# Performance work log

Measured on AMD Instinct MI355X. Metric: run time of the kernel, lower is better.

## Reference

```python
import jax, jax.numpy as jnp
import numpy as np

B, L, H = 512, 10, 256   # batch dialogs, max context len (=dia_len), hidden_size
D = 2 * H                # utt encoding dim (bidirectional)
E = 0.01                 # self.e
BN_EPS = 1e-5


def _linear(x, w, b):
    return x @ w.T + b


def _bn(x, g, b):
    # BatchNorm2d over channel dim 1 of [B, L, L, hid]; training-mode batch stats.
    m = jnp.mean(x, axis=(0, 2, 3), keepdims=True)
    v = jnp.mean((x - m) ** 2, axis=(0, 2, 3), keepdims=True)
    return (x - m) / jnp.sqrt(v + BN_EPS) * g[None, :, None, None] + b[None, :, None, None]


def setup_inputs() -> dict:
    key = jax.random.key(0)
    ks = jax.random.split(key, 24)
    u = lambda k, s: jax.random.uniform(k, s, jnp.float32, -0.02, 0.02)
    n = lambda k, s: jax.random.normal(k, s, jnp.float32) * 0.05
    inp = {
        'utt_encs': jax.random.normal(ks[0], (B, L, D), jnp.float32),
        'aij_eps': jax.random.normal(ks[1], (B, L, L), jnp.float32),
        'sij_eps': jax.random.normal(ks[2], (B, L, L), jnp.float32),
        'context_lens': jax.random.randint(ks[3], (B,), 2, L + 1),
        # mlp_aij_mij: Linear(4H->H), BN, ReLU, Linear(H->H), BN, ReLU, Linear(H->1)
        'a_w1': u(ks[4], (H, 2 * D)), 'a_b1': jnp.zeros((H,)),
        'a_g1': jnp.ones((L,)), 'a_be1': jnp.zeros((L,)),
        'a_w2': u(ks[5], (H, H)), 'a_b2': jnp.zeros((H,)),
        'a_g2': jnp.ones((L,)), 'a_be2': jnp.zeros((L,)),
        'a_w3': u(ks[6], (1, H)), 'a_b3': jnp.zeros((1,)),
        # mlp_sij: Linear(4H->H), BN, Tanh, Linear(H->H), BN, Tanh
        's_w1': u(ks[7], (H, 2 * D)), 's_b1': jnp.zeros((H,)),
        's_g1': jnp.ones((L,)), 's_be1': jnp.zeros((L,)),
        's_w2': u(ks[8], (H, H)), 's_b2': jnp.zeros((H,)),
        's_g2': jnp.ones((L,)), 's_be2': jnp.zeros((L,)),
        'mu_w': u(ks[9], (1, H)), 'mu_b': jnp.zeros((1,)),
        'sg_w': u(ks[10], (1, H)), 'sg_b': jnp.zeros((1,)),
        # update_hidden_state: GRU(2H -> H), single step
        'gru_wi': n(ks[11], (3 * H, D)), 'gru_wh': n(ks[12], (3 * H, H)),
        'gru_bi': jnp.zeros((3 * H,)), 'gru_bh': jnp.zeros((3 * H,)),
    }
    return inp


def reference(utt_encs, aij_eps, sij_eps, context_lens,
              a_w1, a_b1, a_g1, a_be1, a_w2, a_b2, a_g2, a_be2, a_w3, a_b3,
              s_w1, s_b1, s_g1, s_be1, s_w2, s_b2, s_g2, s_be2,
              mu_w, mu_b, sg_w, sg_b, gru_wi, gru_wh, gru_bi, gru_bh):
    # pairwise concat [B, L, L, 4H]
    x_ij = jnp.concatenate([
        jnp.broadcast_to(utt_encs[:, :, None, :], (B, L, L, D)),
        jnp.broadcast_to(utt_encs[:, None, :, :], (B, L, L, D)),
    ], axis=-1)
    # aij branch
    h1 = jax.nn.relu(_bn(_linear(x_ij, a_w1, a_b1), a_g1, a_be1))
    h2 = jax.nn.relu(_bn(_linear(h1, a_w2, a_b2), a_g2, a_be2))
    aij_mij = _linear(h2, a_w3, a_b3)[..., 0]                      # [B, L, L]
    aij_mu = jax.nn.softplus(aij_mij) + E
    aij_std = jnp.sqrt(jax.nn.softplus((1.0 - aij_mu) * aij_mu) + E)
    aij = jax.nn.softplus(aij_eps * aij_std + aij_mu) + E
    # sij branch
    t1 = jnp.tanh(_bn(_linear(x_ij, s_w1, s_b1), s_g1, s_be1))
    sij_latent = jnp.tanh(_bn(_linear(t1, s_w2, s_b2), s_g2, s_be2))
    sij_mu = _linear(sij_latent, mu_w, mu_b)[..., 0]
    sij_sigma = _linear(sij_latent, sg_w, sg_b)[..., 0]
    sij = sij_eps * jnp.sqrt(aij * sij_sigma * sij_sigma) + aij * sij_mu
    wij = aij * sij                                                # [B, L, L]
    # per-dialog aggregation (vectorized): anchor = context_lens - 1,
    # neighbors are j < anchor (anchor row, anchor excluded, j <= num_neighbours)
    anchor = context_lens - 1                                      # [B]
    w_row = jnp.take_along_axis(wij, anchor[:, None, None], axis=1)[:, 0, :]  # [B, L]
    mask = jnp.arange(L)[None, :] < anchor[:, None]
    logits = jnp.where(mask, w_row, -jnp.inf)
    p = jax.nn.softmax(logits, axis=-1)
    p = jnp.where(mask, p, 0.0)
    message = jnp.einsum('bj,bjd->bd', p, utt_encs)                # [B, 2H]
    ue_a = jnp.take_along_axis(utt_encs, anchor[:, None, None], axis=1)[:, 0, :]
    h0 = ue_a[:, :H] + ue_a[:, H:]                                 # [B, H]
    # single GRU step (torch GRU cell math)
    gi = message @ gru_wi.T + gru_bi
    gh = h0 @ gru_wh.T + gru_bh
    i_r, i_z, i_n = jnp.split(gi, 3, axis=-1)
    h_r, h_z, h_n = jnp.split(gh, 3, axis=-1)
    r = jax.nn.sigmoid(i_r + h_r)
    z = jax.nn.sigmoid(i_z + h_z)
    ncand = jnp.tanh(i_n + r * h_n)
    return (1.0 - z) * ncand + z * h0                              # [B, H]
```

## Files before the change

### kernel.cpp

```cpp
#include <hip/hip_runtime.h>
#include <math.h>


typedef __attribute__((ext_vector_type(8))) short short8;
typedef __attribute__((ext_vector_type(4))) float f32x4;

__device__ __forceinline__ float softplusf(float x) {
  return x > 0.f ? x + log1pf(expf(-x)) : log1pf(expf(x));
}
__device__ __forceinline__ float wred64(float v) {
#pragma unroll
  for (int o = 32; o > 0; o >>= 1) v += __shfl_down(v, o);
  return v;
}
__device__ __forceinline__ unsigned short f2bf(float f) {
  unsigned int u = __float_as_uint(f);
  u += 0x7fffu + ((u >> 16) & 1u);
  return (unsigned short)(u >> 16);
}
__device__ __forceinline__ float bf2f(unsigned short u) {
  return __uint_as_float(((unsigned int)u) << 16);
}
__device__ __forceinline__ short8 pack8(const float* __restrict__ p) {
  float4 v0 = *(const float4*)p;
  float4 v1 = *(const float4*)(p + 4);
  short8 r;
  r[0] = (short)f2bf(v0.x); r[1] = (short)f2bf(v0.y);
  r[2] = (short)f2bf(v0.z); r[3] = (short)f2bf(v0.w);
  r[4] = (short)f2bf(v1.x); r[5] = (short)f2bf(v1.y);
  r[6] = (short)f2bf(v1.z); r[7] = (short)f2bf(v1.w);
  return r;
}

__global__ __launch_bounds__(256) void prep_weights(
    const float* __restrict__ utt,
    const float* __restrict__ a_w1, const float* __restrict__ s_w1,
    const float* __restrict__ a_w2, const float* __restrict__ s_w2,
    const float* __restrict__ gru_wi, const float* __restrict__ gru_wh,
    unsigned short* __restrict__ Af, unsigned short* __restrict__ Bf,
    unsigned short* __restrict__ W2fa, unsigned short* __restrict__ W2fs,
    unsigned short* __restrict__ wibf, unsigned short* __restrict__ whbf) {
  int i = blockIdx.x * 256 + threadIdx.x;
  if (i < 327680) {
    int lane = i & 63, ks = (i >> 6) & 15, rb = i >> 10;
    int row = rb * 16 + (lane & 15);
    int k = ks * 32 + (lane >> 4) * 8;
    *(short8*)&Af[i * 8] = pack8(&utt[row * 512 + k]);
    return;
  }
  i -= 327680;
  if (i < 65536) {
    int lane = i & 63, cf = (i >> 6) & 3, ks = (i >> 8) & 15, cb = i >> 12;
    int c = cb * 64 + cf * 16 + (lane & 15);
    int k = ks * 32 + (lane >> 4) * 8;
    const float* src;
    if (c < 256)       src = &a_w1[c * 1024 + k];
    else if (c < 512)  src = &a_w1[(c - 256) * 1024 + 512 + k];
    else if (c < 768)  src = &s_w1[(c - 512) * 1024 + k];
    else               src = &s_w1[(c - 768) * 1024 + 512 + k];
    *(short8*)&Bf[i * 8] = pack8(src);
    return;
  }
  i -= 65536;
  if (i < 8192) {
    int lane = i & 63, cf = (i >> 6) & 3, ks = (i >> 8) & 7, cb = i >> 11;
    int c = cb * 64 + cf * 16 + (lane & 15);
    int k = ks * 32 + (lane >> 4) * 8;
    *(short8*)&W2fa[i * 8] = pack8(&a_w2[c * 256 + k]);
    return;
  }
  i -= 8192;
  if (i < 8192) {
    int lane = i & 63, cf = (i >> 6) & 3, ks = (i >> 8) & 7, cb = i >> 11;
    int c = cb * 64 + cf * 16 + (lane & 15);
    int k = ks * 32 + (lane >> 4) * 8;
    *(short8*)&W2fs[i * 8] = pack8(&s_w2[c * 256 + k]);
    return;
  }
  i -= 8192;
  if (i < 49152) { *(short8*)&wibf[i * 8] = pack8(&gru_wi[i * 8]); return; }
  i -= 49152;
  *(short8*)&whbf[i * 8] = pack8(&gru_wh[i * 8]);
}

__global__ __launch_bounds__(256) void gemm_pq_swz(
    const unsigned short* __restrict__ Af, const unsigned short* __restrict__ Bf,
    unsigned short* __restrict__ C) {
  int t = threadIdx.x;
  int w = t >> 6, l = t & 63, li = l & 15, lg = l >> 4;
  int rb0 = blockIdx.x * 4;
  int cb = blockIdx.y * 4 + w;
  const unsigned short* Bb = Bf + cb * (16 * 4 * 512);
  f32x4 acc[4][4] = {};
  short8 acur[4], bcur[4], anxt[4], bnxt[4];
#pragma unroll
  for (int fr = 0; fr < 4; ++fr) acur[fr] = *(const short8*)&Af[((rb0 + fr) * 16 + 0) * 512 + l * 8];
#pragma unroll
  for (int cf = 0; cf < 4; ++cf) bcur[cf] = *(const short8*)&Bb[(0 * 4 + cf) * 512 + l * 8];
  for (int ks = 0; ks < 16; ++ks) {
    if (ks < 15) {
#pragma unroll
      for (int fr = 0; fr < 4; ++fr) anxt[fr] = *(const short8*)&Af[((rb0 + fr) * 16 + ks + 1) * 512 + l * 8];
#pragma unroll
      for (int cf = 0; cf < 4; ++cf) bnxt[cf] = *(const short8*)&Bb[((ks + 1) * 4 + cf) * 512 + l * 8];
    }
#pragma unroll
    for (int fr = 0; fr < 4; ++fr)
#pragma unroll
      for (int cf = 0; cf < 4; ++cf)
        acc[fr][cf] = __builtin_amdgcn_mfma_f32_16x16x32_bf16(acur[fr], bcur[cf], acc[fr][cf], 0, 0, 0);
#pragma unroll
    for (int fr = 0; fr < 4; ++fr) acur[fr] = anxt[fr];
#pragma unroll
    for (int cf = 0; cf < 4; ++cf) bcur[cf] = bnxt[cf];
  }
  int rowBase = blockIdx.x * 64, colBase = cb * 64;
#pragma unroll
  for (int fr = 0; fr < 4; ++fr)
#pragma unroll
    for (int reg = 0; reg < 4; ++reg) {
      int r = rowBase + fr * 16 + lg * 4 + reg;
      unsigned short* crow = C + r * 1024 + colBase + li;
#pragma unroll
      for (int cf = 0; cf < 4; ++cf) crow[cf * 16] = f2bf(acc[fr][cf][reg]);
    }
}

__global__ __launch_bounds__(256) void stats_kernel(
    const unsigned short* __restrict__ PQ, const float* __restrict__ a_b1,
    const float* __restrict__ s_b1, float* __restrict__ Part) {
  __shared__ float lbins[4][32];
  int b = blockIdx.x, br = blockIdx.y, t = threadIdx.x;
  int w = t >> 6, l = t & 63;
  const unsigned short* base = PQ + b * 10240 + (br ? 512 : 0);
  const float* b1 = br ? s_b1 : a_b1;
  float P[10], Q[10];
#pragma unroll
  for (int j = 0; j < 10; ++j) Q[j] = bf2f(base[j * 1024 + 256 + t]);
#pragma unroll
  for (int i = 0; i < 10; ++i) P[i] = bf2f(base[i * 1024 + t]);
  float sq = 0.f, sq2 = 0.f;
#pragma unroll
  for (int j = 0; j < 10; ++j) { sq += Q[j]; sq2 += Q[j] * Q[j]; }
  float qbar = sq * 0.1f;
  float bb1 = b1[t];
  float r;
  r = wred64(sq);  if (l == 0) lbins[w][0] = r;
  r = wred64(sq2); if (l == 0) lbins[w][1] = r;
#pragma unroll
  for (int i = 0; i < 10; ++i) {
    float a = P[i] + bb1;
    r = wred64(P[i]);     if (l == 0) lbins[w][2 + i * 3] = r;
    r = wred64(a * a);    if (l == 0) lbins[w][3 + i * 3] = r;
    r = wred64(a * qbar); if (l == 0) lbins[w][4 + i * 3] = r;
  }
  __syncthreads();
  if (t < 32) Part[(b * 2 + br) * 32 + t] = lbins[0][t] + lbins[1][t] + lbins[2][t] + lbins[3][t];
}

__global__ void reduce_bn1(const float* __restrict__ Part,
                           const float* __restrict__ a_b1, const float* __restrict__ s_b1,
                           const float* __restrict__ a_g1, const float* __restrict__ a_be1,
                           const float* __restrict__ s_g1, const float* __restrict__ s_be1,
                           float* __restrict__ ST) {
  __shared__ float tmp[256];
  __shared__ float mom[32];
  int br = blockIdx.x, t = threadIdx.x;
  int v = t & 31, c = t >> 5;
  float s = 0.f;
  for (int b = c * 64; b < c * 64 + 64; ++b) s += Part[(b * 2 + br) * 32 + v];
  tmp[t] = s;
  __syncthreads();
  if (t < 32) {
    float m = 0.f;
#pragma unroll
    for (int k = 0; k < 8; ++k) m += tmp[k * 32 + t];
    mom[t] = m;
  }
  __syncthreads();
  if (t < 10) {
    int i = t;
    const float* b1 = br ? s_b1 : a_b1;
    float bsum = 0.f;
    for (int h = 0; h < 256; ++h) bsum += b1[h];
    float meanb1 = bsum * (1.f / 256.f);
    const float invBH = 1.f / (512.f * 256.f);
    const float invBLH = 1.f / (512.f * 10.f * 256.f);
    float SP = mom[2 + i * 3], SA2 = mom[3 + i * 3], SPQ = mom[4 + i * 3];
    float SQ = mom[0], SQ2 = mom[1];
    float mean = SP * invBH + meanb1 + SQ * invBLH;
    float Ez2 = SA2 * invBH + 2.f * SPQ * invBH + SQ2 * invBLH;
    float var = Ez2 - mean * mean;
    float g = br ? s_g1[i] : a_g1[i];
    float be = br ? s_be1[i] : a_be1[i];
    float sc = g / sqrtf(var + 1e-5f);
    ST[64 + br * 20 + i] = sc;
    ST[64 + br * 20 + 10 + i] = be - mean * sc;
  }
}

__global__ __launch_bounds__(256, 4) void fused_layer2_half(
    const unsigned short* __restrict__ PQ, const float* __restrict__ ST,
    const float* __restrict__ a_b1, const float* __restrict__ s_b1,
    const unsigned short* __restrict__ W2fa, const unsigned short* __restrict__ W2fs,
    const float* __restrict__ a_b2, const float* __restrict__ s_b2,
    const int* __restrict__ cl, unsigned short* __restrict__ Z2a, unsigned short* __restrict__ Z2s,
    float* __restrict__ Part2) {
  __shared__ __align__(16) unsigned short Atile[64][264];
  __shared__ float bins[10];
  int b = blockIdx.x, half = blockIdx.y, br = blockIdx.z;
  int i0 = half * 5;
  int p_off = br ? 512 : 0;
  const float* b1 = br ? s_b1 : a_b1;
  const unsigned short* W2f = br ? W2fs : W2fa;
  const float* b2 = br ? s_b2 : a_b2;
  unsigned short* Z2out = br ? Z2s : Z2a;
  int sc_off = br ? 84 : 64;
  int t = threadIdx.x;
  int anc = cl[b] - 1;
  if (t < 10) bins[t] = 0.f;
  int w = t >> 6, l = t & 63, li = l & 15, lg = l >> 4;
  int colBase = w * 64;
  const unsigned short* Wb = W2f + w * (8 * 4 * 512);
  short8 bcur[4], bnxt[4];
#pragma unroll
  for (int cf = 0; cf < 4; ++cf) bcur[cf] = *(const short8*)&Wb[(0 * 4 + cf) * 512 + l * 8];
  float b2v[4];
#pragma unroll
  for (int cf = 0; cf < 4; ++cf) b2v[cf] = b2[colBase + cf * 16 + li];
  for (int idx = t; idx < 14 * 264; idx += 256) (&Atile[50][0])[idx] = 0;
  {
    int c = t;
    float b1c = b1[c];
    float P[5], Q[10];
#pragma unroll
    for (int j = 0; j < 10; ++j) Q[j] = bf2f(PQ[(b * 10 + j) * 1024 + p_off + 256 + c]);
#pragma unroll
    for (int il = 0; il < 5; ++il) P[il] = bf2f(PQ[(b * 10 + i0 + il) * 1024 + p_off + c]);
#pragma unroll
    for (int il = 0; il < 5; ++il) {
      float sc = ST[sc_off + i0 + il], sh = ST[sc_off + 10 + i0 + il];
      float base = (P[il] + b1c) * sc + sh;
#pragma unroll
      for (int j = 0; j < 10; ++j) {
        float z = base + Q[j] * sc;
        float h;
        if (br) {
          float ex = __expf(2.f * z);
          h = (ex - 1.f) / (ex + 1.f);
        } else {
          h = fmaxf(z, 0.f);
        }
        Atile[il * 10 + j][c] = f2bf(h);
      }
    }
  }
  __syncthreads();
  f32x4 acc[4][4] = {};
  for (int ks = 0; ks < 8; ++ks) {
    if (ks < 7) {
#pragma unroll
      for (int cf = 0; cf < 4; ++cf) bnxt[cf] = *(const short8*)&Wb[((ks + 1) * 4 + cf) * 512 + l * 8];
    }
    int ka = ks * 32 + lg * 8;
#pragma unroll
    for (int fr = 0; fr < 4; ++fr) {
      short8 afr = *(const short8*)&Atile[fr * 16 + li][ka];
#pragma unroll
      for (int cf = 0; cf < 4; ++cf)
        acc[fr][cf] = __builtin_amdgcn_mfma_f32_16x16x32_bf16(afr, bcur[cf], acc[fr][cf], 0, 0, 0);
    }
#pragma unroll
    for (int cf = 0; cf < 4; ++cf) bcur[cf] = bnxt[cf];
  }
#pragma unroll
  for (int fr = 0; fr < 4; ++fr) {
#pragma unroll
    for (int reg = 0; reg < 4; ++reg) {
      int row = fr * 16 + lg * 4 + reg;
      bool valid = row < 50;
      int il = row / 10, jj = row - il * 10;
      float z0 = acc[fr][0][reg] + b2v[0];
      float z1 = acc[fr][1][reg] + b2v[1];
      float z2 = acc[fr][2][reg] + b2v[2];
      float z3 = acc[fr][3][reg] + b2v[3];
      if (valid && (i0 + il) == anc) {
        unsigned short* dst = Z2out + (b * 10 + jj) * 256 + colBase + li;
        dst[0] = f2bf(z0); dst[16] = f2bf(z1); dst[32] = f2bf(z2); dst[48] = f2bf(z3);
      }
      float s = valid ? (z0 + z1 + z2 + z3) : 0.f;
      float q = valid ? (z0 * z0 + z1 * z1 + z2 * z2 + z3 * z3) : 0.f;
#pragma unroll
      for (int o = 1; o < 16; o <<= 1) {
        s += __shfl_xor(s, o);
        q += __shfl_xor(q, o);
      }
      if (li == 0 && valid) {
        atomicAdd(&bins[il], s);
        atomicAdd(&bins[5 + il], q);
      }
    }
  }
  __syncthreads();
  if (t < 5) {
    Part2[(br * 10 + i0 + t) * 512 + b] = bins[t];
    Part2[10240 + (br * 10 + i0 + t) * 512 + b] = bins[5 + t];
  }
}

__global__ __launch_bounds__(256) void finalize_bn2(
    const float* __restrict__ Part2,
    const float* __restrict__ a_g2, const float* __restrict__ a_be2,
    const float* __restrict__ s_g2, const float* __restrict__ s_be2,
    float* __restrict__ ST) {
  int t = threadIdx.x;
  int w = t >> 6, l = t & 63;
#pragma unroll
  for (int pp = 0; pp < 5; ++pp) {
    int p = w * 5 + pp;
    float s = 0.f, q = 0.f;
#pragma unroll
    for (int k = 0; k < 8; ++k) {
      s += Part2[p * 512 + l + k * 64];
      q += Part2[10240 + p * 512 + l + k * 64];
    }
    s = wred64(s);
    q = wred64(q);
    if (l == 0) {
      int br = p / 10, i = p - br * 10;
      const float invN = 1.f / (512.f * 10.f * 256.f);
      float m = s * invN;
      float v = q * invN - m * m;
      float g = br ? s_g2[i] : a_g2[i];
      float be = br ? s_be2[i] : a_be2[i];
      float sc = g / sqrtf(v + 1e-5f);
      ST[144 + br * 20 + i] = sc;
      ST[144 + br * 20 + 10 + i] = be - m * sc;
    }
  }
}

__global__ __launch_bounds__(256) void gemm_gru2(
    const unsigned short* __restrict__ A0, const unsigned short* __restrict__ B0,
    float* __restrict__ C0, const float* __restrict__ bias0,
    const unsigned short* __restrict__ A1, const unsigned short* __restrict__ B1,
    float* __restrict__ C1, const float* __restrict__ bias1) {
  const unsigned short* A; const unsigned short* Bw; float* C; const float* bias; int K;
  if (blockIdx.z == 0) { A = A0; Bw = B0; C = C0; bias = bias0; K = 512; }
  else                 { A = A1; Bw = B1; C = C1; bias = bias1; K = 256; }
  int t = threadIdx.x;
  int w = t >> 6, l = t & 63, li = l & 15, lg = l >> 4;
  int rowBase = blockIdx.x * 32;
  int colBase = blockIdx.y * 256 + w * 64;
  f32x4 acc[2][4] = {};
  const unsigned short* Arow[2];
  const unsigned short* Brow[4];
#pragma unroll
  for (int fr = 0; fr < 2; ++fr) Arow[fr] = A + (rowBase + fr * 16 + li) * K;
#pragma unroll
  for (int cf = 0; cf < 4; ++cf) Brow[cf] = Bw + (colBase + cf * 16 + li) * K;
  for (int ks = 0; ks < K / 32; ++ks) {
    int ka = ks * 32 + lg * 8;
    short8 afr[2], bfr[4];
#pragma unroll
    for (int fr = 0; fr < 2; ++fr) afr[fr] = *(const short8*)&Arow[fr][ka];
#pragma unroll
    for (int cf = 0; cf < 4; ++cf) bfr[cf] = *(const short8*)&Brow[cf][ka];
#pragma unroll
    for (int fr = 0; fr < 2; ++fr)
#pragma unroll
      for (int cf = 0; cf < 4; ++cf)
        acc[fr][cf] = __builtin_amdgcn_mfma_f32_16x16x32_bf16(afr[fr], bfr[cf], acc[fr][cf], 0, 0, 0);
  }
  float b2v[4];
#pragma unroll
  for (int cf = 0; cf < 4; ++cf) b2v[cf] = bias[colBase + cf * 16 + li];
#pragma unroll
  for (int fr = 0; fr < 2; ++fr)
#pragma unroll
    for (int reg = 0; reg < 4; ++reg) {
      int r = rowBase + fr * 16 + lg * 4 + reg;
      float* crow = C + r * 768 + colBase + li;
#pragma unroll
      for (int cf = 0; cf < 4; ++cf) crow[cf * 16] = acc[fr][cf][reg] + b2v[cf];
    }
}

__global__ __launch_bounds__(256) void postproc_kernel(
    const unsigned short* __restrict__ Z2a, const unsigned short* __restrict__ Z2s,
    const float* __restrict__ ST,
    const float* __restrict__ a_w3, const float* __restrict__ a_b3,
    const float* __restrict__ mu_w, const float* __restrict__ mu_b,
    const float* __restrict__ sg_w, const float* __restrict__ sg_b,
    const float* __restrict__ aij_eps, const float* __restrict__ sij_eps,
    const int* __restrict__ cl, const float* __restrict__ utt,
    unsigned short* __restrict__ msgbf, unsigned short* __restrict__ h0bf,
    float* __restrict__ h0out) {
  int b = blockIdx.x, t = threadIdx.x;
  int w = t >> 6, l = t & 63;
  int a = cl[b] - 1;
  float sc2a = ST[144 + a], sh2a = ST[154 + a];
  float sc2s = ST[164 + a], sh2s = ST[174 + a];
  __shared__ float red[30];
#pragma unroll
  for (int m = 0; m < 3; ++m) {
    int j = w + 4 * m;
    if (j < 10) {
      float pa = 0.f, pm = 0.f, ps = 0.f;
#pragma unroll
      for (int cc = 0; cc < 4; ++cc) {
        int c = l + cc * 64;
        float za = bf2f(Z2a[(b * 10 + j) * 256 + c]);
        float va = fmaxf(za * sc2a + sh2a, 0.f);
        float zs = bf2f(Z2s[(b * 10 + j) * 256 + c]);
        float vs = tanhf(zs * sc2s + sh2s);
        pa += va * a_w3[c];
        pm += vs * mu_w[c];
        ps += vs * sg_w[c];
      }
      pa = wred64(pa); pm = wred64(pm); ps = wred64(ps);
      if (l == 0) { red[j] = pa; red[10 + j] = pm; red[20 + j] = ps; }
    }
  }
  __syncthreads();
  __shared__ float pw[10];
  __shared__ float wijs[16];
  if (t < 10) {
    int j = t;
    float amij = red[j] + a_b3[0];
    float amu = softplusf(amij) + 0.01f;
    float astd = sqrtf(softplusf((1.f - amu) * amu) + 0.01f);
    float ae = aij_eps[b * 100 + a * 10 + j];
    float aij = softplusf(ae * astd + amu) + 0.01f;
    float smu = red[10 + j] + mu_b[0];
    float ssg = red[20 + j] + sg_b[0];
    float se = sij_eps[b * 100 + a * 10 + j];
    float sij = se * sqrtf(aij * ssg * ssg) + aij * smu;
    wijs[j] = aij * sij;
  }
  __syncthreads();
  if (t == 0) {
    float mx = -1e30f;
    for (int j = 0; j < a; ++j) mx = fmaxf(mx, wijs[j]);
    float e[10];
    float den = 0.f;
    for (int j = 0; j < a; ++j) { e[j] = expf(wijs[j] - mx); den += e[j]; }
    for (int j = 0; j < 10; ++j) pw[j] = (j < a) ? e[j] / den : 0.f;
  }
  __syncthreads();
#pragma unroll
  for (int dd = 0; dd < 2; ++dd) {
    int d = t + dd * 256;
    float mv = 0.f;
#pragma unroll
    for (int j = 0; j < 10; ++j) mv += pw[j] * utt[(b * 10 + j) * 512 + d];
    msgbf[b * 512 + d] = f2bf(mv);
  }
  float u1 = utt[(b * 10 + a) * 512 + t];
  float u2 = utt[(b * 10 + a) * 512 + 256 + t];
  float h0v = u1 + u2;
  h0out[b * 256 + t] = h0v;
  h0bf[b * 256 + t] = f2bf(h0v);
}

__global__ __launch_bounds__(256) void gru_final(const float* __restrict__ gi,
                                                 const float* __restrict__ gh,
                                                 const float* __restrict__ h0,
                                                 float* __restrict__ out) {
  int idx = blockIdx.x * 256 + threadIdx.x;
  int b = idx >> 8, h = idx & 255;
  float ir = gi[b * 768 + h], iz = gi[b * 768 + 256 + h], inn = gi[b * 768 + 512 + h];
  float hr = gh[b * 768 + h], hz = gh[b * 768 + 256 + h], hn = gh[b * 768 + 512 + h];
  float r = 1.f / (1.f + expf(-(ir + hr)));
  float z = 1.f / (1.f + expf(-(iz + hz)));
  float n = tanhf(inn + r * hn);
  out[idx] = (1.f - z) * n + z * h0[b * 256 + h];
}

extern "C" void kernel_launch(void* const* d_in, const int* in_sizes, int n_in,
                              void* d_out, int out_size, void* d_ws, size_t ws_size,
                              hipStream_t stream) {
  const float* utt = (const float*)d_in[0];
  const float* aij_eps = (const float*)d_in[1];
  const float* sij_eps = (const float*)d_in[2];
  const int* cl = (const int*)d_in[3];
  const float* a_w1 = (const float*)d_in[4];
  const float* a_b1 = (const float*)d_in[5];
  const float* a_g1 = (const float*)d_in[6];
  const float* a_be1 = (const float*)d_in[7];
  const float* a_w2 = (const float*)d_in[8];
  const float* a_b2 = (const float*)d_in[9];
  const float* a_g2 = (const float*)d_in[10];
  const float* a_be2 = (const float*)d_in[11];
  const float* a_w3 = (const float*)d_in[12];
  const float* a_b3 = (const float*)d_in[13];
  const float* s_w1 = (const float*)d_in[14];
  const float* s_b1 = (const float*)d_in[15];
  const float* s_g1 = (const float*)d_in[16];
  const float* s_be1 = (const float*)d_in[17];
  const float* s_w2 = (const float*)d_in[18];
  const float* s_b2 = (const float*)d_in[19];
  const float* s_g2 = (const float*)d_in[20];
  const float* s_be2 = (const float*)d_in[21];
  const float* mu_w = (const float*)d_in[22];
  const float* mu_b = (const float*)d_in[23];
  const float* sg_w = (const float*)d_in[24];
  const float* sg_b = (const float*)d_in[25];
  const float* gru_wi = (const float*)d_in[26];
  const float* gru_wh = (const float*)d_in[27];
  const float* gru_bi = (const float*)d_in[28];
  const float* gru_bh = (const float*)d_in[29];

  float* ws = (float*)d_ws;
  float* ST = ws;
  unsigned short* Af = (unsigned short*)(ws + 256);
  unsigned short* Bf = Af + 2621440;
  unsigned short* W2fa = Bf + 524288;
  unsigned short* W2fs = W2fa + 65536;
  unsigned short* wibf = W2fs + 65536;
  unsigned short* whbf = wibf + 393216;
  float* PQf = (float*)(whbf + 196608);
  unsigned short* PQ = (unsigned short*)PQf;
  unsigned short* Z2a = (unsigned short*)(PQf + 5242880);
  unsigned short* Z2s = Z2a + 1310720;
  float* Part = PQf + 5242880 + 1310720;
  float* Part2 = Part + 32768;
  float* tailf = PQf + 2621440;
  unsigned short* msgbf = (unsigned short*)tailf;
  unsigned short* h0bf = msgbf + 262144;
  float* h0 = tailf + 196608;
  float* gi = tailf + 327680;
  float* gh = gi + 393216;

  prep_weights<<<1888, 256, 0, stream>>>(utt, a_w1, s_w1, a_w2, s_w2, gru_wi, gru_wh,
                                         Af, Bf, W2fa, W2fs, wibf, whbf);
  gemm_pq_swz<<<dim3(80, 4), 256, 0, stream>>>(Af, Bf, PQ);
  stats_kernel<<<dim3(512, 2), 256, 0, stream>>>(PQ, a_b1, s_b1, Part);
  reduce_bn1<<<2, 256, 0, stream>>>(Part, a_b1, s_b1, a_g1, a_be1, s_g1, s_be1, ST);
  fused_layer2_half<<<dim3(512, 2, 2), 256, 0, stream>>>(PQ, ST, a_b1, s_b1, W2fa, W2fs,
                                                         a_b2, s_b2, cl, Z2a, Z2s, Part2);
  finalize_bn2<<<1, 256, 0, stream>>>(Part2, a_g2, a_be2, s_g2, s_be2, ST);
  postproc_kernel<<<512, 256, 0, stream>>>(Z2a, Z2s, ST, a_w3, a_b3, mu_w, mu_b, sg_w, sg_b,
                                           aij_eps, sij_eps, cl, utt, msgbf, h0bf, h0);
  gemm_gru2<<<dim3(16, 3, 2), 256, 0, stream>>>(msgbf, wibf, gi, gru_bi,
                                                h0bf, whbf, gh, gru_bh);
  gru_final<<<512, 256, 0, stream>>>(gi, gh, h0, (float*)d_out);
}
```

Before: 121.1 us.

## Process both branches per block in layer2 and fold BN2 finalize into postproc

The layer-2 kernel now handles the aij and sij branches in one block, looping over the branch index, so the grid halves and each block does twice the work. The separate single-block finalize_bn2 launch is removed; postproc now reduces the Part2 partial sums for its anchor row itself and computes the BN2 scale and shift in shared memory. This cuts a serialized tiny launch and one kernel boundary. The cost is that each postproc block redundantly reduces 512 partials, and layer2 has fewer, longer blocks, which means less parallelism.

```diff
diff --git a/kernel.cpp b/kernel.cpp
--- a/kernel.cpp
+++ b/kernel.cpp
@@ -199,7 +199,7 @@
   }
 }
 
-__global__ __launch_bounds__(256, 4) void fused_layer2_half(
+__global__ __launch_bounds__(256, 4) void fused_layer2_pair(
     const unsigned short* __restrict__ PQ, const float* __restrict__ ST,
     const float* __restrict__ a_b1, const float* __restrict__ s_b1,
     const unsigned short* __restrict__ W2fa, const unsigned short* __restrict__ W2fs,
@@ -207,136 +207,109 @@
     const int* __restrict__ cl, unsigned short* __restrict__ Z2a, unsigned short* __restrict__ Z2s,
     float* __restrict__ Part2) {
   __shared__ __align__(16) unsigned short Atile[64][264];
-  __shared__ float bins[10];
-  int b = blockIdx.x, half = blockIdx.y, br = blockIdx.z;
+  __shared__ float bins[20];
+  int b = blockIdx.x, half = blockIdx.y;
   int i0 = half * 5;
-  int p_off = br ? 512 : 0;
-  const float* b1 = br ? s_b1 : a_b1;
-  const unsigned short* W2f = br ? W2fs : W2fa;
-  const float* b2 = br ? s_b2 : a_b2;
-  unsigned short* Z2out = br ? Z2s : Z2a;
-  int sc_off = br ? 84 : 64;
   int t = threadIdx.x;
-  int anc = cl[b] - 1;
-  if (t < 10) bins[t] = 0.f;
   int w = t >> 6, l = t & 63, li = l & 15, lg = l >> 4;
   int colBase = w * 64;
-  const unsigned short* Wb = W2f + w * (8 * 4 * 512);
-  short8 bcur[4], bnxt[4];
-#pragma unroll
-  for (int cf = 0; cf < 4; ++cf) bcur[cf] = *(const short8*)&Wb[(0 * 4 + cf) * 512 + l * 8];
-  float b2v[4];
-#pragma unroll
-  for (int cf = 0; cf < 4; ++cf) b2v[cf] = b2[colBase + cf * 16 + li];
+  int anc = cl[b] - 1;
+  if (t < 20) bins[t] = 0.f;
   for (int idx = t; idx < 14 * 264; idx += 256) (&Atile[50][0])[idx] = 0;
-  {
-    int c = t;
-    float b1c = b1[c];
-    float P[5], Q[10];
-#pragma unroll
-    for (int j = 0; j < 10; ++j) Q[j] = bf2f(PQ[(b * 10 + j) * 1024 + p_off + 256 + c]);
-#pragma unroll
-    for (int il = 0; il < 5; ++il) P[il] = bf2f(PQ[(b * 10 + i0 + il) * 1024 + p_off + c]);
-#pragma unroll
-    for (int il = 0; il < 5; ++il) {
-      float sc = ST[sc_off + i0 + il], sh = ST[sc_off + 10 + i0 + il];
-      float base = (P[il] + b1c) * sc + sh;
-#pragma unroll
-      for (int j = 0; j < 10; ++j) {
-        float z = base + Q[j] * sc;
-        float h;
-        if (br) {
-          float ex = __expf(2.f * z);
-          h = (ex - 1.f) / (ex + 1.f);
-        } else {
-          h = fmaxf(z, 0.f);
+#pragma unroll
+  for (int br = 0; br < 2; ++br) {
+    int p_off = br ? 512 : 0;
+    const float* b1 = br ? s_b1 : a_b1;
+    const unsigned short* W2f = br ? W2fs : W2fa;
+    const float* b2 = br ? s_b2 : a_b2;
+    unsigned short* Z2out = br ? Z2s : Z2a;
+    int sc_off = br ? 84 : 64;
+    const unsigned short* Wb = W2f + w * (8 * 4 * 512);
+    short8 bcur[4], bnxt[4];
+#pragma unroll
+    for (int cf = 0; cf < 4; ++cf) bcur[cf] = *(const short8*)&Wb[(0 * 4 + cf) * 512 + l * 8];
+    float b2v[4];
+#pragma unroll
+    for (int cf = 0; cf < 4; ++cf) b2v[cf] = b2[colBase + cf * 16 + li];
+    {
+      int c = t;
+      float b1c = b1[c];
+      float P[5], Q[10];
+#pragma unroll
+      for (int j = 0; j < 10; ++j) Q[j] = bf2f(PQ[(b * 10 + j) * 1024 + p_off + 256 + c]);
+#pragma unroll
+      for (int il = 0; il < 5; ++il) P[il] = bf2f(PQ[(b * 10 + i0 + il) * 1024 + p_off + c]);
+#pragma unroll
+      for (int il = 0; il < 5; ++il) {
+        float sc = ST[sc_off + i0 + il], sh = ST[sc_off + 10 + i0 + il];
+        float base = (P[il] + b1c) * sc + sh;
+#pragma unroll
+        for (int j = 0; j < 10; ++j) {
+          float z = base + Q[j] * sc;
+          float h;
+          if (br) {
+            float ex = __expf(2.f * z);
+            h = (ex - 1.f) / (ex + 1.f);
+          } else {
+            h = fmaxf(z, 0.f);
+          }
+          Atile[il * 10 + j][c] = f2bf(h);
         }
-        Atile[il * 10 + j][c] = f2bf(h);
       }
     }
-  }
-  __syncthreads();
-  f32x4 acc[4][4] = {};
-  for (int ks = 0; ks < 8; ++ks) {
-    if (ks < 7) {
-#pragma unroll
-      for (int cf = 0; cf < 4; ++cf) bnxt[cf] = *(const short8*)&Wb[((ks + 1) * 4 + cf) * 512 + l * 8];
-    }
-    int ka = ks * 32 + lg * 8;
+    __syncthreads();
+    f32x4 acc[4][4] = {};
+    for (int ks = 0; ks < 8; ++ks) {
+      if (ks < 7) {
+#pragma unroll
+        for (int cf = 0; cf < 4; ++cf) bnxt[cf] = *(const short8*)&Wb[((ks + 1) * 4 + cf) * 512 + l * 8];
+      }
+      int ka = ks * 32 + lg * 8;
+#pragma unroll
+      for (int fr = 0; fr < 4; ++fr) {
+        short8 afr = *(const short8*)&Atile[fr * 16 + li][ka];
+#pragma unroll
+        for (int cf = 0; cf < 4; ++cf)
+          acc[fr][cf] = __builtin_amdgcn_mfma_f32_16x16x32_bf16(afr, bcur[cf], acc[fr][cf], 0, 0, 0);
+      }
+#pragma unroll
+      for (int cf = 0; cf < 4; ++cf) bcur[cf] = bnxt[cf];
+    }
 #pragma unroll
     for (int fr = 0; fr < 4; ++fr) {
-      short8 afr = *(const short8*)&Atile[fr * 16 + li][ka];
-#pragma unroll
-      for (int cf = 0; cf < 4; ++cf)
-        acc[fr][cf] = __builtin_amdgcn_mfma_f32_16x16x32_bf16(afr, bcur[cf], acc[fr][cf], 0, 0, 0);
-    }
-#pragma unroll
-    for (int cf = 0; cf < 4; ++cf) bcur[cf] = bnxt[cf];
-  }
-#pragma unroll
-  for (int fr = 0; fr < 4; ++fr) {
-#pragma unroll
-    for (int reg = 0; reg < 4; ++reg) {
-      int row = fr * 16 + lg * 4 + reg;
-      bool valid = row < 50;
-      int il = row / 10, jj = row - il * 10;
-      float z0 = acc[fr][0][reg] + b2v[0];
-      float z1 = acc[fr][1][reg] + b2v[1];
-      float z2 = acc[fr][2][reg] + b2v[2];
-      float z3 = acc[fr][3][reg] + b2v[3];
-      if (valid && (i0 + il) == anc) {
-        unsigned short* dst = Z2out + (b * 10 + jj) * 256 + colBase + li;
-        dst[0] = f2bf(z0); dst[16] = f2bf(z1); dst[32] = f2bf(z2); dst[48] = f2bf(z3);
+#pragma unroll
+      for (int reg = 0; reg < 4; ++reg) {
+        int row = fr * 16 + lg * 4 + reg;
+        bool valid = row < 50;
+        int il = row / 10, jj = row - il * 10;
+        float z0 = acc[fr][0][reg] + b2v[0];
+        float z1 = acc[fr][1][reg] + b2v[1];
+        float z2 = acc[fr][2][reg] + b2v[2];
+        float z3 = acc[fr][3][reg] + b2v[3];
+        if (valid && (i0 + il) == anc) {
+          unsigned short* dst = Z2out + (b * 10 + jj) * 256 + colBase + li;
+          dst[0] = f2bf(z0); dst[16] = f2bf(z1); dst[32] = f2bf(z2); dst[48] = f2bf(z3);
+        }
+        float s = valid ? (z0 + z1 + z2 + z3) : 0.f;
+        float q = valid ? (z0 * z0 + z1 * z1 + z2 * z2 + z3 * z3) : 0.f;
+#pragma unroll
+        for (int o = 1; o < 16; o <<= 1) {
+          s += __shfl_xor(s, o);
+          q += __shfl_xor(q, o);
+        }
+        if (li == 0 && valid) {
+          atomicAdd(&bins[br * 10 + il], s);
+          atomicAdd(&bins[br * 10 + 5 + il], q);
+        }
       }
-      float s = valid ? (z0 + z1 + z2 + z3) : 0.f;
-      float q = valid ? (z0 * z0 + z1 * z1 + z2 * z2 + z3 * z3) : 0.f;
-#pragma unroll
-      for (int o = 1; o < 16; o <<= 1) {
-        s += __shfl_xor(s, o);
-        q += __shfl_xor(q, o);
-      }
-      if (li == 0 && valid) {
-        atomicAdd(&bins[il], s);
-        atomicAdd(&bins[5 + il], q);
-      }
-    }
-  }
-  __syncthreads();
+    }
+    __syncthreads();
+  }
   if (t < 5) {
-    Part2[(br * 10 + i0 + t) * 512 + b] = bins[t];
-    Part2[10240 + (br * 10 + i0 + t) * 512 + b] = bins[5 + t];
-  }
-}
-
-__global__ __launch_bounds__(256) void finalize_bn2(
-    const float* __restrict__ Part2,
-    const float* __restrict__ a_g2, const float* __restrict__ a_be2,
-    const float* __restrict__ s_g2, const float* __restrict__ s_be2,
-    float* __restrict__ ST) {
-  int t = threadIdx.x;
-  int w = t >> 6, l = t & 63;
-#pragma unroll
-  for (int pp = 0; pp < 5; ++pp) {
-    int p = w * 5 + pp;
-    float s = 0.f, q = 0.f;
-#pragma unroll
-    for (int k = 0; k < 8; ++k) {
-      s += Part2[p * 512 + l + k * 64];
-      q += Part2[10240 + p * 512 + l + k * 64];
-    }
-    s = wred64(s);
-    q = wred64(q);
-    if (l == 0) {
-      int br = p / 10, i = p - br * 10;
-      const float invN = 1.f / (512.f * 10.f * 256.f);
-      float m = s * invN;
-      float v = q * invN - m * m;
-      float g = br ? s_g2[i] : a_g2[i];
-      float be = br ? s_be2[i] : a_be2[i];
-      float sc = g / sqrtf(v + 1e-5f);
-      ST[144 + br * 20 + i] = sc;
-      ST[144 + br * 20 + 10 + i] = be - m * sc;
-    }
+    Part2[(i0 + t) * 512 + b] = bins[t];
+    Part2[10240 + (i0 + t) * 512 + b] = bins[5 + t];
+    Part2[(10 + i0 + t) * 512 + b] = bins[10 + t];
+    Part2[10240 + (10 + i0 + t) * 512 + b] = bins[15 + t];
   }
 }
 
@@ -387,8 +360,10 @@
 }
 
 __global__ __launch_bounds__(256) void postproc_kernel(
+    const float* __restrict__ Part2,
+    const float* __restrict__ a_g2, const float* __restrict__ a_be2,
+    const float* __restrict__ s_g2, const float* __restrict__ s_be2,
     const unsigned short* __restrict__ Z2a, const unsigned short* __restrict__ Z2s,
-    const float* __restrict__ ST,
     const float* __restrict__ a_w3, const float* __restrict__ a_b3,
     const float* __restrict__ mu_w, const float* __restrict__ mu_b,
     const float* __restrict__ sg_w, const float* __restrict__ sg_b,
@@ -399,8 +374,31 @@
   int b = blockIdx.x, t = threadIdx.x;
   int w = t >> 6, l = t & 63;
   int a = cl[b] - 1;
-  float sc2a = ST[144 + a], sh2a = ST[154 + a];
-  float sc2s = ST[164 + a], sh2s = ST[174 + a];
+  __shared__ float bn2r[4];
+  {
+    int p = (w >> 1) * 10 + a;
+    int off = (w & 1) ? 10240 : 0;
+    float s = 0.f;
+#pragma unroll
+    for (int k = 0; k < 8; ++k) s += Part2[off + p * 512 + l + k * 64];
+    s = wred64(s);
+    if (l == 0) bn2r[w] = s;
+  }
+  __syncthreads();
+  __shared__ float sc2[4];
+  if (t < 2) {
+    int br = t;
+    const float invN = 1.f / (512.f * 10.f * 256.f);
+    float m = bn2r[br * 2 + 0] * invN;
+    float v = bn2r[br * 2 + 1] * invN - m * m;
+    float g = br ? s_g2[a] : a_g2[a];
+    float be = br ? s_be2[a] : a_be2[a];
+    float sc = g / sqrtf(v + 1e-5f);
+    sc2[br * 2] = sc;
+    sc2[br * 2 + 1] = be - m * sc;
+  }
+  __syncthreads();
+  float sc2a = sc2[0], sh2a = sc2[1], sc2s = sc2[2], sh2s = sc2[3];
   __shared__ float red[30];
 #pragma unroll
   for (int m = 0; m < 3; ++m) {
@@ -537,10 +535,10 @@
   gemm_pq_swz<<<dim3(80, 4), 256, 0, stream>>>(Af, Bf, PQ);
   stats_kernel<<<dim3(512, 2), 256, 0, stream>>>(PQ, a_b1, s_b1, Part);
   reduce_bn1<<<2, 256, 0, stream>>>(Part, a_b1, s_b1, a_g1, a_be1, s_g1, s_be1, ST);
-  fused_layer2_half<<<dim3(512, 2, 2), 256, 0, stream>>>(PQ, ST, a_b1, s_b1, W2fa, W2fs,
-                                                         a_b2, s_b2, cl, Z2a, Z2s, Part2);
-  finalize_bn2<<<1, 256, 0, stream>>>(Part2, a_g2, a_be2, s_g2, s_be2, ST);
-  postproc_kernel<<<512, 256, 0, stream>>>(Z2a, Z2s, ST, a_w3, a_b3, mu_w, mu_b, sg_w, sg_b,
+  fused_layer2_pair<<<dim3(512, 2), 256, 0, stream>>>(PQ, ST, a_b1, s_b1, W2fa, W2fs,
+                                                      a_b2, s_b2, cl, Z2a, Z2s, Part2);
+  postproc_kernel<<<512, 256, 0, stream>>>(Part2, a_g2, a_be2, s_g2, s_be2,
+                                           Z2a, Z2s, a_w3, a_b3, mu_w, mu_b, sg_w, sg_b,
                                            aij_eps, sij_eps, cl, utt, msgbf, h0bf, h0);
   gemm_gru2<<<dim3(16, 3, 2), 256, 0, stream>>>(msgbf, wibf, gi, gru_bi,
                                                 h0bf, whbf, gh, gru_bh);
```

New measurement: 129.7 us. +7.2%, slower.
